# Performance work log

Measured on AMD Instinct MI355X. Metric: run time of the kernel, lower is better.

The kernel has to match this reference:

```python
import jax, jax.numpy as jnp
import numpy as np
from jax.scipy.special import logsumexp

B, S, H, T = 64, 512, 768, 9

def setup_inputs() -> dict:
    key = jax.random.key(0)
    ks = jax.random.split(key, 6)
    return {
        "encoder_out": jax.random.normal(ks[0], (B, S, H), jnp.float32),
        "labels": jax.random.randint(ks[1], (B, S), 0, T, jnp.int32),
        "mask": jnp.ones((B, S), jnp.int32),
        "lengths": jnp.full((B,), S, jnp.int32),
        "fc_w": jax.random.normal(ks[2], (T, H), jnp.float32) * 0.02,
        "fc_b": jnp.zeros((T,), jnp.float32),
        "start_trans": jax.random.uniform(ks[3], (T,), jnp.float32, -0.1, 0.1),
        "end_trans": jax.random.uniform(ks[4], (T,), jnp.float32, -0.1, 0.1),
        "trans": jax.random.uniform(ks[5], (T, T), jnp.float32, -0.1, 0.1),
    }

def crf_log_likelihood(em, tg, mk, start, end, trans):
    # em: [S,B,T], tg: [S,B], mk: [S,B] float. torchcrf forward (reduction='none').
    barange = jnp.arange(em.shape[1])
    # --- numerator: score of the gold path ---
    score0 = start[tg[0]] + em[0][barange, tg[0]]
    def num_step(carry, x):
        score, prev = carry
        em_i, tg_i, mk_i = x
        score = score + (trans[prev, tg_i] + em_i[barange, tg_i]) * mk_i
        prev = jnp.where(mk_i > 0, tg_i, prev)
        return (score, prev), None
    (score, prev), _ = jax.lax.scan(num_step, (score0, tg[0]), (em[1:], tg[1:], mk[1:]))
    numerator = score + end[prev]
    # --- denominator: log partition via forward algorithm ---
    alpha = start[None, :] + em[0]  # [B,T]
    def den_step(alpha, x):
        em_i, mk_i = x
        nxt = logsumexp(alpha[:, :, None] + trans[None] + em_i[:, None, :], axis=1)
        return jnp.where(mk_i[:, None] > 0, nxt, alpha), None
    alpha, _ = jax.lax.scan(den_step, alpha, (em[1:], mk[1:]))
    denominator = logsumexp(alpha + end[None, :], axis=1)
    return numerator - denominator  # [B]

def crf_viterbi(em, mk, start, end, trans):
    # em: [S,B,T], mk: [S,B] float. Returns best path [S,B].
    barange = jnp.arange(em.shape[1])
    alpha = start[None, :] + em[0]  # [B,T]
    idT = jnp.arange(em.shape[2])[None, :]
    def fwd_step(alpha, x):
        em_i, mk_i = x
        scores = alpha[:, :, None] + trans[None]  # [B, T_prev, T_cur]
        bp = jnp.argmax(scores, axis=1)           # [B,T]
        nxt = jnp.max(scores, axis=1) + em_i
        valid = mk_i[:, None] > 0
        return jnp.where(valid, nxt, alpha), jnp.where(valid, bp, idT)
    alpha, bps = jax.lax.scan(fwd_step, alpha, (em[1:], mk[1:]))  # bps: [S-1,B,T]
    last = jnp.argmax(alpha + end[None, :], axis=1)  # [B]
    def back_step(tag, bp):
        prev = bp[barange, tag]
        return prev, prev
    _, path_head = jax.lax.scan(back_step, last, bps, reverse=True)  # [S-1,B]
    return jnp.concatenate([path_head, last[None, :]], axis=0)  # [S,B]

def reference(encoder_out, labels, mask, lengths, fc_w, fc_b, start_trans, end_trans, trans):
    # dropout in eval mode == identity
    emissions = jnp.einsum('bsh,th->bst', encoder_out, fc_w) + fc_b  # [B,S,T]
    em = jnp.swapaxes(emissions, 0, 1)               # [S,B,T]
    tg = jnp.swapaxes(labels, 0, 1)                  # [S,B]
    mk = jnp.swapaxes(mask, 0, 1).astype(emissions.dtype)
    ll = crf_log_likelihood(em, tg, mk, start_trans, end_trans, trans)  # [B]
    ner_loss = jnp.mean(-ll)
    path = crf_viterbi(em, mk, start_trans, end_trans, trans)  # [S,B]
    ner_predict = jnp.swapaxes(path, 0, 1)  # [B,S]
    return ner_loss, ner_predict, lengths
```

## Files before the change

kernel.cpp:

```cpp
#include <hip/hip_runtime.h>

#define Bsz 64
#define Ssz 512
#define Hsz 768
#define Tsz 9
#define NCH 16
#define LOG2E 1.4426950408889634f
#define LN2F  0.6931471805599453f

__device__ __forceinline__ int SK(int s) { return s * Tsz + ((s >> 5) << 1); }

__global__ __launch_bounds__(256) void emis_kernel(
    const float* __restrict__ x, const float* __restrict__ fcw,
    const float* __restrict__ fcb, float* __restrict__ em) {
    __shared__ float4 w4[Tsz * Hsz / 4];
    __shared__ float bias[Tsz];
    __shared__ float part[16 * Tsz * 16];
    const int tid = threadIdx.x;
    const float4* fw4 = reinterpret_cast<const float4*>(fcw);
#pragma unroll
    for (int i = 0; i < 7; ++i) {
        const int o = tid + i * 256;
        if (o < 1728) w4[o] = fw4[o];
    }
    if (tid < Tsz) bias[tid] = fcb[tid];
    __syncthreads();

    const int p = tid >> 4, l = tid & 15;
    const float4* xr = reinterpret_cast<const float4*>(
        x + ((size_t)blockIdx.x * 16 + p) * Hsz);
    float acc[Tsz];
#pragma unroll
    for (int t = 0; t < Tsz; ++t) acc[t] = 0.0f;
#pragma unroll
    for (int i = 0; i < 12; ++i) {
        const float4 xv = xr[i * 16 + l];
#pragma unroll
        for (int t = 0; t < Tsz; ++t) {
            const float4 wv = w4[t * 192 + i * 16 + l];
            acc[t] = fmaf(xv.x, wv.x, fmaf(xv.y, wv.y,
                     fmaf(xv.z, wv.z, fmaf(xv.w, wv.w, acc[t]))));
        }
    }
#pragma unroll
    for (int t = 0; t < Tsz; ++t) part[(p * Tsz + t) * 16 + l] = acc[t];
    __syncthreads();
    if (tid < 16 * Tsz) {
        const int t = tid % Tsz;
        float s = bias[t];
#pragma unroll
        for (int l2 = 0; l2 < 16; ++l2) s += part[tid * 16 + l2];
        em[(size_t)blockIdx.x * (16 * Tsz) + tid] = s;
    }
}

__global__ __launch_bounds__(256, 1) void pass1_kernel(
    const float* __restrict__ em, const int* __restrict__ mask,
    const float* __restrict__ trans, float* __restrict__ R2,
    float* __restrict__ MV) {
    const int tid = threadIdx.x;
    if (blockIdx.x < 36) {
        const int flat = blockIdx.x * 256 + tid;
        const int a = flat % Tsz;
        const int bc = flat / Tsz;
        const int c = bc & 15;
        const int b = bc >> 4;

        float E[81];
#pragma unroll
        for (int i = 0; i < 81; ++i) E[i] = exp2f(trans[i] * LOG2E);

        float pp[Tsz];
#pragma unroll
        for (int j = 0; j < Tsz; ++j) pp[j] = (j == a) ? 1.0f : 0.0f;
        float K = 0.0f;

        const float* emb = em + (size_t)b * Ssz * Tsz;
        const int* mkb = mask + b * Ssz;
        const int s_lo = c * 32 + 1;
        const int s_hi = min(c * 32 + 32, Ssz - 1);

        float ec[Tsz];
#pragma unroll
        for (int j = 0; j < Tsz; ++j) ec[j] = emb[s_lo * Tsz + j];
        int mc = mkb[s_lo];

        for (int s = s_lo; s <= s_hi; ++s) {
            const int sp = (s < s_hi) ? s + 1 : s;
            float en[Tsz];
#pragma unroll
            for (int j = 0; j < Tsz; ++j) en[j] = emb[sp * Tsz + j];
            const int mn = mkb[sp];

            float g[Tsz];
#pragma unroll
            for (int j = 0; j < Tsz; ++j) g[j] = pp[0] * E[j];
#pragma unroll
            for (int i = 1; i < Tsz; ++i)
#pragma unroll
                for (int j = 0; j < Tsz; ++j) g[j] = fmaf(pp[i], E[i * Tsz + j], g[j]);
#pragma unroll
            for (int j = 0; j < Tsz; ++j) {
                const float ex = exp2f(ec[j] * LOG2E);
                const float np = g[j] * ex;
                if (mc > 0) pp[j] = np;
            }
            if (((s - s_lo) & 7) == 7) {
                float ss = 0.0f;
#pragma unroll
                for (int j = 0; j < Tsz; ++j) ss += pp[j];
                K += __log2f(ss);
                const float inv = 1.0f / ss;
#pragma unroll
                for (int j = 0; j < Tsz; ++j) pp[j] *= inv;
            }
#pragma unroll
            for (int j = 0; j < Tsz; ++j) ec[j] = en[j];
            mc = mn;
        }
        float* outp = R2 + ((size_t)bc * Tsz + a) * Tsz;
#pragma unroll
        for (int j = 0; j < Tsz; ++j) outp[j] = K + __log2f(pp[j]);
    } else {
        const int flat = (blockIdx.x - 36) * 256 + tid;
        const int a = flat % Tsz;
        const int bc = flat / Tsz;
        const int c = bc & 15;
        const int b = bc >> 4;

        float T[81];
#pragma unroll
        for (int i = 0; i < 81; ++i) T[i] = trans[i];

        float row[Tsz];
#pragma unroll
        for (int j = 0; j < Tsz; ++j) row[j] = (j == a) ? 0.0f : -1e30f;

        const float* emb = em + (size_t)b * Ssz * Tsz;
        const int* mkb = mask + b * Ssz;
        const int s_lo = c * 32 + 1;
        const int s_hi = min(c * 32 + 32, Ssz - 1);

        float ec[Tsz];
#pragma unroll
        for (int j = 0; j < Tsz; ++j) ec[j] = emb[s_lo * Tsz + j];
        int mc = mkb[s_lo];

        for (int s = s_lo; s <= s_hi; ++s) {
            const int sp = (s < s_hi) ? s + 1 : s;
            float en[Tsz];
#pragma unroll
            for (int j = 0; j < Tsz; ++j) en[j] = emb[sp * Tsz + j];
            const int mn = mkb[sp];

            float g[Tsz];
#pragma unroll
            for (int j = 0; j < Tsz; ++j) g[j] = row[0] + T[j];
#pragma unroll
            for (int i = 1; i < Tsz; ++i)
#pragma unroll
                for (int j = 0; j < Tsz; ++j) g[j] = fmaxf(g[j], row[i] + T[i * Tsz + j]);
#pragma unroll
            for (int j = 0; j < Tsz; ++j)
                if (mc > 0) row[j] = g[j] + ec[j];
#pragma unroll
            for (int j = 0; j < Tsz; ++j) ec[j] = en[j];
            mc = mn;
        }
        float* o = MV + (size_t)bc * 81 + a * Tsz;
#pragma unroll
        for (int j = 0; j < Tsz; ++j) o[j] = row[j];
    }
}

__device__ __forceinline__ void amax9(const float (&v)[Tsz], float& bv, int& bi) {
    float w01v = (v[1] > v[0]) ? v[1] : v[0]; int w01i = (v[1] > v[0]) ? 1 : 0;
    float w23v = (v[3] > v[2]) ? v[3] : v[2]; int w23i = (v[3] > v[2]) ? 3 : 2;
    float w45v = (v[5] > v[4]) ? v[5] : v[4]; int w45i = (v[5] > v[4]) ? 5 : 4;
    float w67v = (v[7] > v[6]) ? v[7] : v[6]; int w67i = (v[7] > v[6]) ? 7 : 6;
    float x03v = (w23v > w01v) ? w23v : w01v; int x03i = (w23v > w01v) ? w23i : w01i;
    float x47v = (w67v > w45v) ? w67v : w45v; int x47i = (w67v > w45v) ? w67i : w45i;
    float y07v = (x47v > x03v) ? x47v : x03v; int y07i = (x47v > x03v) ? x47i : x03i;
    bv = (v[8] > y07v) ? v[8] : y07v;
    bi = (v[8] > y07v) ? 8 : y07i;
}

__global__ __launch_bounds__(192, 1) void vit3_kernel(
    const float* __restrict__ em, const int* __restrict__ labels,
    const int* __restrict__ mask, const float* __restrict__ start_t,
    const float* __restrict__ end_t, const float* __restrict__ trans,
    const float* __restrict__ R2, const float* __restrict__ MV,
    float* __restrict__ out_path, float* __restrict__ ll) {
    __shared__ __align__(16) float em_s[4640];
    __shared__ __align__(16) int   mk_s[Ssz];
    __shared__ __align__(16) float mv_s[NCH * 81];
    __shared__ __align__(16) float r2_s[NCH * 81];
    __shared__ float tr_s[81];
    __shared__ float st_s[12], en_s[12];
    __shared__ __align__(16) float alc[2][NCH][12];
    __shared__ float a2c[2][12];
    __shared__ unsigned char bp[(Ssz - 1) * Tsz];
    __shared__ unsigned char mapA[64][12], mapB[64][12];
    __shared__ float den_sh, num_sh;

    const int b = blockIdx.x, tid = threadIdx.x;
    const int wv = tid >> 6, ln = tid & 63;
    const int c = tid / 12, j9 = tid % 12;
    const float* emb = em + (size_t)b * Ssz * Tsz;
    const int* mkb = mask + b * Ssz;
    const int* lbb = labels + b * Ssz;

    for (int i = tid; i < Ssz * Tsz; i += 192) {
        const int s = i / 9, j = i - s * 9;
        em_s[SK(s) + j] = emb[i];
    }
    for (int i = tid; i < Ssz; i += 192) mk_s[i] = mkb[i];
    {
        const float4* v4 = reinterpret_cast<const float4*>(MV + (size_t)b * NCH * 81);
        float4* vd = reinterpret_cast<float4*>(mv_s);
        for (int i = tid; i < NCH * 81 / 4; i += 192) vd[i] = v4[i];
        const float4* r4 = reinterpret_cast<const float4*>(R2 + (size_t)b * NCH * 81);
        float4* rd = reinterpret_cast<float4*>(r2_s);
        for (int i = tid; i < NCH * 81 / 4; i += 192) rd[i] = r4[i];
        if (tid < 81) tr_s[tid] = trans[tid];
        if (tid >= 96 && tid < 96 + Tsz) {
            st_s[tid - 96] = start_t[tid - 96];
            en_s[tid - 96] = end_t[tid - 96];
        }
    }
    __syncthreads();

    float tc[Tsz];
    const int jj = (j9 < Tsz) ? j9 : Tsz - 1;
#pragma unroll
    for (int i = 0; i < Tsz; ++i) tc[i] = tr_s[i * Tsz + jj];

    float aj = 0.0f;
    if (c == 0 && j9 < Tsz) {
        aj = st_s[j9] + em_s[j9];
        alc[0][0][j9] = aj;
    }
    if (wv == 1 && ln < Tsz) a2c[0][ln] = (st_s[ln] + em_s[ln]) * LOG2E;

    for (int r = 0; r < NCH; ++r) {
        __syncthreads();
        if (r < NCH - 1 && c == r + 1 && j9 < Tsz) {
            const float* M = &mv_s[r * 81];
            float m = alc[0][r][0] + M[j9];
#pragma unroll
            for (int i = 1; i < Tsz; ++i)
                m = fmaxf(m, alc[0][r][i] + M[i * Tsz + j9]);
            aj = m;
            alc[0][c][j9] = m;
        }
        if (wv == 1 && ln < Tsz) {
            const float* Rr = &r2_s[r * 81];
            float xi[Tsz];
#pragma unroll
            for (int i = 0; i < Tsz; ++i) xi[i] = a2c[r & 1][i] + Rr[i * Tsz + ln];
            float m = xi[0];
#pragma unroll
            for (int i = 1; i < Tsz; ++i) m = fmaxf(m, xi[i]);
            float sm = 0.0f;
#pragma unroll
            for (int i = 0; i < Tsz; ++i) sm += exp2f(xi[i] - m);
            a2c[(r + 1) & 1][ln] = m + __log2f(sm);
        }
    }

    int pb = 0;
    for (int k = 0; k < 32; ++k) {
        __syncthreads();
        const int s = c * 32 + 1 + k;
        if (j9 < Tsz && s <= Ssz - 1) {
            const int mk = mk_s[s];
            float av[12];
            const float4* ap = reinterpret_cast<const float4*>(&alc[pb][c][0]);
            *reinterpret_cast<float4*>(&av[0]) = ap[0];
            *reinterpret_cast<float4*>(&av[4]) = ap[1];
            *reinterpret_cast<float4*>(&av[8]) = ap[2];
            float v[Tsz];
#pragma unroll
            for (int i = 0; i < Tsz; ++i) v[i] = av[i] + tc[i];
            float bv; int bi;
            amax9(v, bv, bi);
            bp[(s - 1) * Tsz + j9] = (unsigned char)((mk > 0) ? bi : j9);
            if (mk > 0) aj = bv + em_s[SK(s) + j9];
        }
        if (j9 < Tsz) alc[1 - pb][c][j9] = aj;
        pb ^= 1;
    }
    __syncthreads();

    float bb = alc[0][NCH - 1][0] + en_s[0];
    int last = 0;
#pragma unroll
    for (int q = 1; q < Tsz; ++q) {
        const float qq = alc[0][NCH - 1][q] + en_s[q];
        if (qq > bb) { bb = qq; last = q; }
    }

    const int lo = ln * 8;
    const int hi = min(lo + 7, Ssz - 2);
    if (wv == 0) {
        int xf[Tsz];
#pragma unroll
        for (int t = 0; t < Tsz; ++t) xf[t] = t;
        for (int k = hi; k >= lo; --k) {
#pragma unroll
            for (int t = 0; t < Tsz; ++t) xf[t] = bp[k * Tsz + xf[t]];
        }
#pragma unroll
        for (int t = 0; t < Tsz; ++t) mapA[ln][t] = (unsigned char)xf[t];
    } else if (wv == 1) {
        if (ln == 0) {
            float xv[Tsz];
#pragma unroll
            for (int i = 0; i < Tsz; ++i) xv[i] = a2c[0][i] + en_s[i] * LOG2E;
            float m = xv[0];
#pragma unroll
            for (int i = 1; i < Tsz; ++i) m = fmaxf(m, xv[i]);
            float sm = 0.0f;
#pragma unroll
            for (int i = 0; i < Tsz; ++i) sm += exp2f(xv[i] - m);
            den_sh = m + __log2f(sm);
        }
    } else {
        float part = 0.0f;
        for (int s = 1 + ln; s < Ssz; s += 64) {
            if (mk_s[s] > 0) {
                const int tg = lbb[s];
                int pq = s - 1;
                while (pq > 0 && mk_s[pq] == 0) --pq;
                part += tr_s[lbb[pq] * Tsz + tg] + em_s[SK(s) + tg];
            }
        }
#pragma unroll
        for (int off = 32; off >= 1; off >>= 1) part += __shfl_xor(part, off, 64);
        if (ln == 0) {
            const int tg0 = lbb[0];
            float num = part + st_s[tg0] + em_s[tg0];
            int pq = Ssz - 1;
            while (pq > 0 && mk_s[pq] == 0) --pq;
            num += en_s[lbb[pq]];
            num_sh = num;
        }
    }

#define VIT_RND(CUR, NXT, D)                                               \
    {                                                                      \
        unsigned char nn[Tsz];                                             \
        if (wv == 0) {                                                     \
            const int o = ln + (D);                                        \
            if (o < 64) {                                                  \
                _Pragma("unroll") for (int t = 0; t < Tsz; ++t)            \
                    nn[t] = CUR[ln][CUR[o][t]];                            \
            } else {                                                       \
                _Pragma("unroll") for (int t = 0; t < Tsz; ++t)            \
                    nn[t] = CUR[ln][t];                                    \
            }                                                              \
        }                                                                  \
        __syncthreads();                                                   \
        if (wv == 0) {                                                     \
            _Pragma("unroll") for (int t = 0; t < Tsz; ++t)                \
                NXT[ln][t] = nn[t];                                        \
        }                                                                  \
        __syncthreads();                                                   \
    }
    VIT_RND(mapA, mapB, 1)
    VIT_RND(mapB, mapA, 2)
    VIT_RND(mapA, mapB, 4)
    VIT_RND(mapB, mapA, 8)
    VIT_RND(mapA, mapB, 16)
    VIT_RND(mapB, mapA, 32)
#undef VIT_RND

    if (wv == 0) {
        int t = (ln == 63) ? last : (int)mapA[ln + 1][last];
        float* op = out_path + (size_t)b * Ssz;
        for (int k = hi; k >= lo; --k) {
            t = bp[k * Tsz + t];
            op[k] = (float)t;
        }
        if (ln == 0) op[Ssz - 1] = (float)last;
    }
    if (tid == 0) ll[b] = num_sh - den_sh * LN2F;
}

__global__ __launch_bounds__(64) void fin2_kernel(const float* __restrict__ ll,
                                                  const int* __restrict__ lengths,
                                                  float* __restrict__ dout) {
    const int lane = threadIdx.x;
    float v = ll[lane];
#pragma unroll
    for (int off = 32; off >= 1; off >>= 1) v += __shfl_xor(v, off, 64);
    if (lane == 0) dout[0] = -v * (1.0f / (float)Bsz);
    dout[1 + Bsz * Ssz + lane] = (float)lengths[lane];
}

extern "C" void kernel_launch(void* const* d_in, const int* in_sizes, int n_in,
                              void* d_out, int out_size, void* d_ws, size_t ws_size,
                              hipStream_t stream) {
    const float* enc    = (const float*)d_in[0];
    const int*   labels = (const int*)d_in[1];
    const int*   mask   = (const int*)d_in[2];
    const int*   lengths= (const int*)d_in[3];
    const float* fcw    = (const float*)d_in[4];
    const float* fcb    = (const float*)d_in[5];
    const float* startt = (const float*)d_in[6];
    const float* endt   = (const float*)d_in[7];
    const float* trans  = (const float*)d_in[8];

    float* out = (float*)d_out;
    float* em  = (float*)d_ws;
    float* R2  = em + (size_t)Bsz * Ssz * Tsz;
    float* MV  = R2 + (size_t)Bsz * NCH * 81;
    float* ll  = MV + (size_t)Bsz * NCH * 81;

    emis_kernel<<<Bsz * Ssz / 16, 256, 0, stream>>>(enc, fcw, fcb, em);
    pass1_kernel<<<72, 256, 0, stream>>>(em, mask, trans, R2, MV);
    vit3_kernel<<<Bsz, 192, 0, stream>>>(em, labels, mask, startt, endt, trans,
                                         R2, MV, out + 1, ll);
    fin2_kernel<<<1, 64, 0, stream>>>(ll, lengths, out);
}
```

Measured before the change: 65.35 us.

## Fuse emission GEMV with chunk scan, fold final reduction into Viterbi kernel

The emission projection and the per-chunk forward/Viterbi scans now share one kernel. Each block computes emissions for a 32-step chunk (plus one halo row) into shared memory, then two waves run the logsumexp and max-plus chunk scans straight from LDS while the other waves write the emissions to global memory. The separate loss-reduction kernel is removed: the last Viterbi block, found with an atomic counter, does the mean. This cuts two launches and a global round trip, at the cost of the chunk scans running serially after each block's GEMV on only 18 threads, with 1024 blocks.

```diff
diff --git a/kernel.cpp b/kernel.cpp
--- a/kernel.cpp
+++ b/kernel.cpp
@@ -5,18 +5,29 @@
 #define Hsz 768
 #define Tsz 9
 #define NCH 16
+#define CHW 32
 #define LOG2E 1.4426950408889634f
 #define LN2F  0.6931471805599453f
 
 __device__ __forceinline__ int SK(int s) { return s * Tsz + ((s >> 5) << 1); }
 
-__global__ __launch_bounds__(256) void emis_kernel(
+__global__ __launch_bounds__(256, 1) void emscan_kernel(
     const float* __restrict__ x, const float* __restrict__ fcw,
-    const float* __restrict__ fcb, float* __restrict__ em) {
-    __shared__ float4 w4[Tsz * Hsz / 4];
+    const float* __restrict__ fcb, const int* __restrict__ mask,
+    const float* __restrict__ trans, float* __restrict__ em,
+    float* __restrict__ R2, float* __restrict__ MV, int* __restrict__ cnt) {
+    __shared__ __align__(16) float4 w4[Tsz * Hsz / 4];
     __shared__ float bias[Tsz];
-    __shared__ float part[16 * Tsz * 16];
+    __shared__ float em_w[33 * Tsz];
+    __shared__ int mk_w[33];
+
     const int tid = threadIdx.x;
+    const int bc = blockIdx.x;
+    const int b = bc >> 4, c = bc & 15;
+    const int base = c * CHW;
+
+    if (bc == 0 && tid == 0) *cnt = 0;
+
     const float4* fw4 = reinterpret_cast<const float4*>(fcw);
 #pragma unroll
     for (int i = 0; i < 7; ++i) {
@@ -24,74 +35,61 @@
         if (o < 1728) w4[o] = fw4[o];
     }
     if (tid < Tsz) bias[tid] = fcb[tid];
+    if (tid < 33) {
+        const int s = base + tid;
+        mk_w[tid] = (s < Ssz) ? mask[b * Ssz + s] : 0;
+    }
     __syncthreads();
 
-    const int p = tid >> 4, l = tid & 15;
-    const float4* xr = reinterpret_cast<const float4*>(
-        x + ((size_t)blockIdx.x * 16 + p) * Hsz);
-    float acc[Tsz];
-#pragma unroll
-    for (int t = 0; t < Tsz; ++t) acc[t] = 0.0f;
-#pragma unroll
-    for (int i = 0; i < 12; ++i) {
-        const float4 xv = xr[i * 16 + l];
-#pragma unroll
-        for (int t = 0; t < Tsz; ++t) {
-            const float4 wv = w4[t * 192 + i * 16 + l];
-            acc[t] = fmaf(xv.x, wv.x, fmaf(xv.y, wv.y,
-                     fmaf(xv.z, wv.z, fmaf(xv.w, wv.w, acc[t]))));
-        }
-    }
-#pragma unroll
-    for (int t = 0; t < Tsz; ++t) part[(p * Tsz + t) * 16 + l] = acc[t];
+    const int l = tid & 7;
+    {
+        const int r = tid >> 3;
+        int rr = r;
+        int extra = 0;
+        do {
+            const float4* xr = reinterpret_cast<const float4*>(
+                x + ((size_t)b * Ssz + base + rr) * Hsz);
+            float acc[Tsz];
+#pragma unroll
+            for (int t = 0; t < Tsz; ++t) acc[t] = 0.0f;
+#pragma unroll 4
+            for (int i = 0; i < 24; ++i) {
+                const float4 xv = xr[i * 8 + l];
+#pragma unroll
+                for (int t = 0; t < Tsz; ++t) {
+                    const float4 wv = w4[t * 192 + i * 8 + l];
+                    acc[t] = fmaf(xv.x, wv.x, fmaf(xv.y, wv.y,
+                             fmaf(xv.z, wv.z, fmaf(xv.w, wv.w, acc[t]))));
+                }
+            }
+#pragma unroll
+            for (int t = 0; t < Tsz; ++t) {
+                acc[t] += __shfl_xor(acc[t], 1, 64);
+                acc[t] += __shfl_xor(acc[t], 2, 64);
+                acc[t] += __shfl_xor(acc[t], 4, 64);
+            }
+#pragma unroll
+            for (int t = 0; t < 8; ++t)
+                if (l == t) em_w[rr * Tsz + t] = acc[t] + bias[t];
+            if (l == 0) em_w[rr * Tsz + 8] = acc[8] + bias[8];
+            extra = (!extra && tid >= 192 && tid < 200 && base + CHW < Ssz);
+            rr = CHW;
+        } while (extra);
+    }
     __syncthreads();
-    if (tid < 16 * Tsz) {
-        const int t = tid % Tsz;
-        float s = bias[t];
-#pragma unroll
-        for (int l2 = 0; l2 < 16; ++l2) s += part[tid * 16 + l2];
-        em[(size_t)blockIdx.x * (16 * Tsz) + tid] = s;
-    }
-}
-
-__global__ __launch_bounds__(256, 1) void pass1_kernel(
-    const float* __restrict__ em, const int* __restrict__ mask,
-    const float* __restrict__ trans, float* __restrict__ R2,
-    float* __restrict__ MV) {
-    const int tid = threadIdx.x;
-    if (blockIdx.x < 36) {
-        const int flat = blockIdx.x * 256 + tid;
-        const int a = flat % Tsz;
-        const int bc = flat / Tsz;
-        const int c = bc & 15;
-        const int b = bc >> 4;
-
+
+    const int wv = tid >> 6, ln = tid & 63;
+    if (wv == 0 && ln < Tsz) {
         float E[81];
 #pragma unroll
         for (int i = 0; i < 81; ++i) E[i] = exp2f(trans[i] * LOG2E);
-
         float pp[Tsz];
 #pragma unroll
-        for (int j = 0; j < Tsz; ++j) pp[j] = (j == a) ? 1.0f : 0.0f;
+        for (int j = 0; j < Tsz; ++j) pp[j] = (j == ln) ? 1.0f : 0.0f;
         float K = 0.0f;
-
-        const float* emb = em + (size_t)b * Ssz * Tsz;
-        const int* mkb = mask + b * Ssz;
-        const int s_lo = c * 32 + 1;
-        const int s_hi = min(c * 32 + 32, Ssz - 1);
-
-        float ec[Tsz];
-#pragma unroll
-        for (int j = 0; j < Tsz; ++j) ec[j] = emb[s_lo * Tsz + j];
-        int mc = mkb[s_lo];
-
-        for (int s = s_lo; s <= s_hi; ++s) {
-            const int sp = (s < s_hi) ? s + 1 : s;
-            float en[Tsz];
-#pragma unroll
-            for (int j = 0; j < Tsz; ++j) en[j] = emb[sp * Tsz + j];
-            const int mn = mkb[sp];
-
+        for (int k = 1; k <= CHW; ++k) {
+            if (base + k >= Ssz) break;
+            const int mk = mk_w[k];
             float g[Tsz];
 #pragma unroll
             for (int j = 0; j < Tsz; ++j) g[j] = pp[0] * E[j];
@@ -101,11 +99,10 @@
                 for (int j = 0; j < Tsz; ++j) g[j] = fmaf(pp[i], E[i * Tsz + j], g[j]);
 #pragma unroll
             for (int j = 0; j < Tsz; ++j) {
-                const float ex = exp2f(ec[j] * LOG2E);
-                const float np = g[j] * ex;
-                if (mc > 0) pp[j] = np;
+                const float np = g[j] * exp2f(em_w[k * Tsz + j] * LOG2E);
+                if (mk > 0) pp[j] = np;
             }
-            if (((s - s_lo) & 7) == 7) {
+            if ((k & 7) == 0) {
                 float ss = 0.0f;
 #pragma unroll
                 for (int j = 0; j < Tsz; ++j) ss += pp[j];
@@ -114,62 +111,39 @@
 #pragma unroll
                 for (int j = 0; j < Tsz; ++j) pp[j] *= inv;
             }
-#pragma unroll
-            for (int j = 0; j < Tsz; ++j) ec[j] = en[j];
-            mc = mn;
-        }
-        float* outp = R2 + ((size_t)bc * Tsz + a) * Tsz;
-#pragma unroll
-        for (int j = 0; j < Tsz; ++j) outp[j] = K + __log2f(pp[j]);
-    } else {
-        const int flat = (blockIdx.x - 36) * 256 + tid;
-        const int a = flat % Tsz;
-        const int bc = flat / Tsz;
-        const int c = bc & 15;
-        const int b = bc >> 4;
-
+        }
+        float* o = R2 + ((size_t)bc * Tsz + ln) * Tsz;
+#pragma unroll
+        for (int j = 0; j < Tsz; ++j) o[j] = K + __log2f(pp[j]);
+    } else if (wv == 1 && ln < Tsz) {
         float T[81];
 #pragma unroll
         for (int i = 0; i < 81; ++i) T[i] = trans[i];
-
         float row[Tsz];
 #pragma unroll
-        for (int j = 0; j < Tsz; ++j) row[j] = (j == a) ? 0.0f : -1e30f;
-
-        const float* emb = em + (size_t)b * Ssz * Tsz;
-        const int* mkb = mask + b * Ssz;
-        const int s_lo = c * 32 + 1;
-        const int s_hi = min(c * 32 + 32, Ssz - 1);
-
-        float ec[Tsz];
-#pragma unroll
-        for (int j = 0; j < Tsz; ++j) ec[j] = emb[s_lo * Tsz + j];
-        int mc = mkb[s_lo];
-
-        for (int s = s_lo; s <= s_hi; ++s) {
-            const int sp = (s < s_hi) ? s + 1 : s;
-            float en[Tsz];
-#pragma unroll
-            for (int j = 0; j < Tsz; ++j) en[j] = emb[sp * Tsz + j];
-            const int mn = mkb[sp];
-
+        for (int j = 0; j < Tsz; ++j) row[j] = (j == ln) ? 0.0f : -1e30f;
+        for (int k = 1; k <= CHW; ++k) {
+            if (base + k >= Ssz) break;
+            const int mk = mk_w[k];
             float g[Tsz];
 #pragma unroll
             for (int j = 0; j < Tsz; ++j) g[j] = row[0] + T[j];
 #pragma unroll
-            for (int i = 1; i < Tsz; ++i)
-#pragma unroll
-                for (int j = 0; j < Tsz; ++j) g[j] = fmaxf(g[j], row[i] + T[i * Tsz + j]);
+            for (int i = 1; i < Tsz; i += 2)
+#pragma unroll
+                for (int j = 0; j < Tsz; ++j)
+                    g[j] = fmaxf(fmaxf(g[j], row[i] + T[i * Tsz + j]),
+                                 row[i + 1] + T[(i + 1) * Tsz + j]);
 #pragma unroll
             for (int j = 0; j < Tsz; ++j)
-                if (mc > 0) row[j] = g[j] + ec[j];
-#pragma unroll
-            for (int j = 0; j < Tsz; ++j) ec[j] = en[j];
-            mc = mn;
-        }
-        float* o = MV + (size_t)bc * 81 + a * Tsz;
+                if (mk > 0) row[j] = g[j] + em_w[k * Tsz + j];
+        }
+        float* o = MV + (size_t)bc * 81 + ln * Tsz;
 #pragma unroll
         for (int j = 0; j < Tsz; ++j) o[j] = row[j];
+    } else if (wv >= 2) {
+        float* eg = em + ((size_t)b * Ssz + base) * Tsz;
+        for (int i = tid - 128; i < CHW * Tsz; i += 128) eg[i] = em_w[i];
     }
 }
 
@@ -187,10 +161,11 @@
 
 __global__ __launch_bounds__(192, 1) void vit3_kernel(
     const float* __restrict__ em, const int* __restrict__ labels,
-    const int* __restrict__ mask, const float* __restrict__ start_t,
-    const float* __restrict__ end_t, const float* __restrict__ trans,
-    const float* __restrict__ R2, const float* __restrict__ MV,
-    float* __restrict__ out_path, float* __restrict__ ll) {
+    const int* __restrict__ mask, const int* __restrict__ lengths,
+    const float* __restrict__ start_t, const float* __restrict__ end_t,
+    const float* __restrict__ trans, const float* __restrict__ R2,
+    const float* __restrict__ MV, float* __restrict__ out_path,
+    float* __restrict__ ll, float* __restrict__ dout, int* __restrict__ cnt) {
     __shared__ __align__(16) float em_s[4640];
     __shared__ __align__(16) int   mk_s[Ssz];
     __shared__ __align__(16) float mv_s[NCH * 81];
@@ -202,6 +177,7 @@
     __shared__ unsigned char bp[(Ssz - 1) * Tsz];
     __shared__ unsigned char mapA[64][12], mapB[64][12];
     __shared__ float den_sh, num_sh;
+    __shared__ int lastf;
 
     const int b = blockIdx.x, tid = threadIdx.x;
     const int wv = tid >> 6, ln = tid & 63;
@@ -384,18 +360,21 @@
         }
         if (ln == 0) op[Ssz - 1] = (float)last;
     }
-    if (tid == 0) ll[b] = num_sh - den_sh * LN2F;
-}
-
-__global__ __launch_bounds__(64) void fin2_kernel(const float* __restrict__ ll,
-                                                  const int* __restrict__ lengths,
-                                                  float* __restrict__ dout) {
-    const int lane = threadIdx.x;
-    float v = ll[lane];
-#pragma unroll
-    for (int off = 32; off >= 1; off >>= 1) v += __shfl_xor(v, off, 64);
-    if (lane == 0) dout[0] = -v * (1.0f / (float)Bsz);
-    dout[1 + Bsz * Ssz + lane] = (float)lengths[lane];
+    if (b == 0 && wv == 2) dout[1 + Bsz * Ssz + ln] = (float)lengths[ln];
+
+    if (tid == 0) {
+        ll[b] = num_sh - den_sh * LN2F;
+        __threadfence();
+        lastf = (atomicAdd(cnt, 1) == Bsz - 1) ? 1 : 0;
+    }
+    __syncthreads();
+    if (lastf && wv == 0) {
+        __threadfence();
+        float v = ll[ln];
+#pragma unroll
+        for (int off = 32; off >= 1; off >>= 1) v += __shfl_xor(v, off, 64);
+        if (ln == 0) dout[0] = -v * (1.0f / (float)Bsz);
+    }
 }
 
 extern "C" void kernel_launch(void* const* d_in, const int* in_sizes, int n_in,
@@ -416,10 +395,10 @@
     float* R2  = em + (size_t)Bsz * Ssz * Tsz;
     float* MV  = R2 + (size_t)Bsz * NCH * 81;
     float* ll  = MV + (size_t)Bsz * NCH * 81;
-
-    emis_kernel<<<Bsz * Ssz / 16, 256, 0, stream>>>(enc, fcw, fcb, em);
-    pass1_kernel<<<72, 256, 0, stream>>>(em, mask, trans, R2, MV);
-    vit3_kernel<<<Bsz, 192, 0, stream>>>(em, labels, mask, startt, endt, trans,
-                                         R2, MV, out + 1, ll);
-    fin2_kernel<<<1, 64, 0, stream>>>(ll, lengths, out);
+    int*   cnt = (int*)(ll + Bsz);
+
+    emscan_kernel<<<Bsz * NCH, 256, 0, stream>>>(enc, fcw, fcb, mask, trans,
+                                                 em, R2, MV, cnt);
+    vit3_kernel<<<Bsz, 192, 0, stream>>>(em, labels, mask, lengths, startt, endt,
+                                         trans, R2, MV, out + 1, ll, out, cnt);
 }
```

Measured after the change: 82.28 us. +25.9%, slower.
